# Kernel optimization log

Measured on AMD Instinct MI355X. Metric: run time of the kernel, lower is better.

Reference implementation:

```python
import jax, jax.numpy as jnp
import numpy as np

# Static module hyperparameters (from init_kwargs)
K = 4        # kernel_size
STRIDE = 2
L = 2        # n_layers
F = 4        # filters
NQ = 6       # n_qubits = ceil(log2(4*4*4)) = 6
D = 1 << NQ  # statevector dim = 64 = in_channels*K*K (no padding needed)

# Pauli-Z expectation sign table: wire 0 is the most-significant bit (PennyLane convention)
_bits = (jnp.arange(D)[None, :] >> (NQ - 1 - jnp.arange(NQ)[:, None])) & 1  # (NQ, D)
ZSIGNS = (1 - 2 * _bits).astype(jnp.float32)                                # (NQ, D)


def setup_inputs() -> dict:
    key = jax.random.key(0)
    k1, k2 = jax.random.split(key)
    x = jax.random.normal(k1, (128, 4, 64, 64), dtype=jnp.float32)
    weights = jax.random.normal(k2, (F, L, NQ, 3), dtype=jnp.float32)
    return {"x": x, "weights": weights}


def _rot_mat(phi, theta, omega):
    # qml.Rot = RZ(omega) @ RY(theta) @ RZ(phi)
    c = jnp.cos(theta / 2)
    s = jnp.sin(theta / 2)
    return jnp.stack([
        jnp.stack([jnp.exp(-1j * (phi + omega) / 2) * c, -jnp.exp(1j * (phi - omega) / 2) * s]),
        jnp.stack([jnp.exp(-1j * (phi - omega) / 2) * s, jnp.exp(1j * (phi + omega) / 2) * c]),
    ])  # (2,2) complex64


def _apply_1q(state, U, w):
    # state: (N, D) complex; apply 2x2 unitary on wire w (MSB-first ordering)
    N = state.shape[0]
    s = state.reshape(N, 1 << w, 2, 1 << (NQ - 1 - w))
    s = jnp.einsum('ij,najb->naib', U, s)
    return s.reshape(N, D)


def _apply_cnot(state, c, t):
    # flip target bit t where control bit c is 1
    N = state.shape[0]
    a, b = min(c, t), max(c, t)
    s = state.reshape(N, 1 << a, 2, 1 << (b - a - 1), 2, 1 << (NQ - 1 - b))
    if c < t:
        # control axis=2, target axis=4
        s = s.at[:, :, 1].set(s[:, :, 1, :, ::-1, :])
    else:
        # target axis=2, control axis=4
        s = s.at[:, :, :, :, 1, :].set(s[:, :, ::-1, :, 1, :])
    return s.reshape(N, D)


def _simulate(psi0, wf):
    # psi0: (N, D) complex64 normalized amplitudes; wf: (L, NQ, 3) float32
    state = psi0
    # The torch module applies StronglyEntanglingLayers(weights) L times -> L*L layers total.
    for _ in range(L):
        for l in range(L):
            for w in range(NQ):
                U = _rot_mat(wf[l, w, 0], wf[l, w, 1], wf[l, w, 2])
                state = _apply_1q(state, U, w)
            r = (l % (NQ - 1)) + 1  # StronglyEntanglingLayers default ranges
            for w in range(NQ):
                state = _apply_cnot(state, w, (w + r) % NQ)
    probs = state.real ** 2 + state.imag ** 2  # (N, D)
    return probs @ ZSIGNS.T                    # (N, NQ) Pauli-Z expvals


def reference(x, weights):
    B, C, H, W = x.shape
    oh = (H - K) // STRIDE + 1
    i = jnp.arange(oh) * STRIDE
    # vectorized sliding-window patch extraction, row-major (i outer, j inner)
    rows = x[:, :, i[:, None] + jnp.arange(K)[None, :], :]           # (B,C,oh,K,W)
    pat = rows[:, :, :, :, i[:, None] + jnp.arange(K)[None, :]]      # (B,C,oh,K,oh,K)
    pat = pat.transpose(0, 2, 4, 1, 3, 5).reshape(B, oh * oh, C * K * K)  # (B,P,D), flatten order (C,k,k)
    # AmplitudeEmbedding with normalize=True (C*K*K == 2**NQ, no padding)
    norm = jnp.linalg.norm(pat, axis=-1, keepdims=True)
    psi0 = (pat / norm).astype(jnp.complex64).reshape(-1, D)         # (B*P, D)
    exp = jax.vmap(lambda wf: _simulate(psi0, wf))(weights)          # (F, B*P, NQ)
    out = exp.reshape(F, B, oh * oh, NQ).transpose(1, 0, 3, 2).reshape(B, F * NQ, oh, oh)
    return out
```

## Files before the change

### kernel.cpp

```cpp
#include <hip/hip_runtime.h>

typedef float f32x2 __attribute__((ext_vector_type(2)));
typedef float f32x16 __attribute__((ext_vector_type(16)));
typedef __bf16 bf16x8 __attribute__((ext_vector_type(8)));

static __device__ __forceinline__ unsigned short f2bf(float v) {
    unsigned u = __builtin_bit_cast(unsigned, v);
    unsigned r = (u + 0x7FFFu + ((u >> 16) & 1u)) >> 16;
    return (unsigned short)r;
}
static __device__ __forceinline__ float bf2f(unsigned short h) {
    unsigned u = ((unsigned)h) << 16;
    return __builtin_bit_cast(float, u);
}
static __device__ __forceinline__ bf16x8 ldg8(const unsigned short* p) {
    uint4 u = *(const uint4*)p;
    return __builtin_bit_cast(bf16x8, u);
}
static __device__ __forceinline__ f32x16 mfma32(bf16x8 a, bf16x8 b, f32x16 c) {
    return __builtin_amdgcn_mfma_f32_32x32x16_bf16(a, b, c, 0, 0, 0);
}

__global__ __launch_bounds__(256) void prep_M(const float* __restrict__ wts,
                                              unsigned short* __restrict__ Mhi) {
    __shared__ float gls[12][8];
    const int f = blockIdx.x >> 4;
    const int tid = threadIdx.x;
    if (tid < 12) {
        int l = tid / 6, w = tid % 6;
        const float* p = wts + ((f * 2 + l) * 6 + w) * 3;
        float phi = p[0], theta = p[1], omega = p[2];
        float c, s; sincosf(0.5f * theta, &s, &c);
        float sapo, capo, samo, camo;
        sincosf(0.5f * (phi + omega), &sapo, &capo);
        sincosf(0.5f * (phi - omega), &samo, &camo);
        float* o = gls[tid];
        o[0] =  capo * c;  o[1] = -sapo * c;
        o[2] = -camo * s;  o[3] = -samo * s;
        o[4] =  camo * s;  o[5] = -samo * s;
        o[6] =  capo * c;  o[7] =  sapo * c;
    }
    __syncthreads();

    const int lane = tid & 63;
    const int wid  = tid >> 6;
    const int bas  = (blockIdx.x & 15) * 4 + wid;

    int src0 = lane, src1 = lane;
#pragma unroll
    for (int w = 5; w >= 0; --w) { int tq = (w + 1) % 6; src0 ^= ((src0 >> (5 - w)) & 1) << (5 - tq); }
#pragma unroll
    for (int w = 5; w >= 0; --w) { int tq = (w + 2) % 6; src1 ^= ((src1 >> (5 - w)) & 1) << (5 - tq); }

    float ar = (lane == bas) ? 1.0f : 0.0f, ai = 0.0f;
#pragma unroll
    for (int rep = 0; rep < 2; ++rep) {
#pragma unroll
        for (int l = 0; l < 2; ++l) {
#pragma unroll
            for (int w = 0; w < 6; ++w) {
                const float* gp = gls[l * 6 + w];
                const float4 uA = *(const float4*)gp;
                const float4 uB = *(const float4*)(gp + 4);
                const int m = 32 >> w;
                const float br = __shfl_xor(ar, m);
                const float bi = __shfl_xor(ai, m);
                const bool hi = (lane & m) != 0;
                const float cmr = hi ? uB.z : uA.x;
                const float cmi = hi ? uB.w : uA.y;
                const float cpr = hi ? uB.x : uA.z;
                const float cpi = hi ? uB.y : uA.w;
                const float nr = cmr * ar - cmi * ai + cpr * br - cpi * bi;
                const float ni = cmr * ai + cmi * ar + cpr * bi + cpi * br;
                ar = nr; ai = ni;
            }
            const int src = l ? src1 : src0;
            ar = __shfl(ar, src);
            ai = __shfl(ai, src);
        }
    }
    Mhi[((f * 2 + 0) * 64 + lane) * 64 + bas] = f2bf(ar);
    Mhi[((f * 2 + 1) * 64 + lane) * 64 + bas] = f2bf(ai);
}

__global__ __launch_bounds__(256, 4) void qconv_main(
        const float* __restrict__ x,
        const unsigned short* __restrict__ Mhi,
        float* __restrict__ out) {
    __shared__ __align__(16) unsigned char smem[12288];
    unsigned short* psiH = (unsigned short*)smem;
    float* zbuf = (float*)smem;

    const int tid  = threadIdx.x;
    const int lane = tid & 63;
    const int w    = tid >> 6;
    const int n0   = blockIdx.x * 64;

    {
        const int p = tid >> 2;
        const int q = tid & 3;
        const int n = n0 + p;
        const int b = n / 961, pos = n - b * 961;
        const int i = pos / 31, j = pos - i * 31;
        const float* base = x + (((b * 4 + q) * 64) + i * 2) * 64 + j * 2;
        float v[16];
#pragma unroll
        for (int kh = 0; kh < 4; ++kh) {
            const float* r = base + kh * 64;
            *(f32x2*)&v[kh * 4]     = *(const f32x2*)r;
            *(f32x2*)&v[kh * 4 + 2] = *(const f32x2*)(r + 2);
        }
        float ss = 0.f;
#pragma unroll
        for (int k = 0; k < 16; ++k) ss += v[k] * v[k];
        ss += __shfl_xor(ss, 1);
        ss += __shfl_xor(ss, 2);
        const float rn = rsqrtf(ss);
        unsigned hu[8];
#pragma unroll
        for (int k2 = 0; k2 < 8; ++k2) {
            __bf16 h0 = (__bf16)(v[2 * k2] * rn);
            __bf16 h1 = (__bf16)(v[2 * k2 + 1] * rn);
            hu[k2] = (unsigned)__builtin_bit_cast(unsigned short, h0)
                   | ((unsigned)__builtin_bit_cast(unsigned short, h1) << 16);
        }
        const int s0i = p * 64 + ((2 * q) ^ (p & 7)) * 8;
        const int s1i = p * 64 + ((2 * q + 1) ^ (p & 7)) * 8;
        *(uint4*)&psiH[s0i] = make_uint4(hu[0], hu[1], hu[2], hu[3]);
        *(uint4*)&psiH[s1i] = make_uint4(hu[4], hu[5], hu[6], hu[7]);
    }
    __syncthreads();

    bf16x8 Bh[2][4];
    {
        const int pc = lane & 31, hi = lane >> 5;
#pragma unroll
        for (int ct = 0; ct < 2; ++ct) {
            const int pp = ct * 32 + pc;
#pragma unroll
            for (int ks = 0; ks < 4; ++ks) {
                const int idx = pp * 64 + ((2 * ks + hi) ^ (pp & 7)) * 8;
                Bh[ct][ks] = __builtin_bit_cast(bf16x8, *(const uint4*)&psiH[idx]);
            }
        }
    }
    __syncthreads();

    const int arow = ((lane >> 4) & 1) * 4096 + (w * 16 + (lane & 15)) * 64 + (lane >> 5) * 8;
    const int hi5 = lane >> 5;

#pragma unroll 1
    for (int fp = 0; fp < 2; ++fp) {
        bf16x8 A8[2][4];
#pragma unroll
        for (int fo = 0; fo < 2; ++fo) {
            const int off = (fp * 2 + fo) * 8192 + arow;
#pragma unroll
            for (int ks = 0; ks < 4; ++ks) A8[fo][ks] = ldg8(Mhi + off + ks * 16);
        }
#pragma unroll
        for (int fo = 0; fo < 2; ++fo) {
            f32x16 C0, C1;
#pragma unroll
            for (int r = 0; r < 16; ++r) { C0[r] = 0.f; C1[r] = 0.f; }
#pragma unroll
            for (int ks = 0; ks < 4; ++ks) {
                C0 = mfma32(A8[fo][ks], Bh[0][ks], C0);
                C1 = mfma32(A8[fo][ks], Bh[1][ks], C1);
            }
#pragma unroll
            for (int ct = 0; ct < 2; ++ct) {
                const f32x16 Cv = ct ? C1 : C0;
                float P[8];
#pragma unroll
                for (int r = 0; r < 8; ++r) P[r] = Cv[r] * Cv[r] + Cv[r + 8] * Cv[r + 8];
                const float e0 = P[0] + P[1], o0 = P[0] - P[1];
                const float e1 = P[2] + P[3], o1 = P[2] - P[3];
                const float e2 = P[4] + P[5], o2 = P[4] - P[5];
                const float e3 = P[6] + P[7], o3 = P[6] - P[7];
                const float s01 = e0 + e1, s23 = e2 + e3;
                float S  = s01 + s23;
                float Z2 = s01 - s23;
                float Z4 = (e0 - e1) + (e2 - e3);
                float Z5 = o0 + o1 + o2 + o3;
                float Z3 = hi5 ? -S : S;
                S  += __shfl_xor(S, 32);
                Z2 += __shfl_xor(Z2, 32);
                Z3 += __shfl_xor(Z3, 32);
                Z4 += __shfl_xor(Z4, 32);
                Z5 += __shfl_xor(Z5, 32);
                if (lane < 32) {
                    const int pp = ct * 32 + lane;
                    zbuf[((fo * 6 + 0) * 4 + w) * 64 + pp] = (w & 2) ? -S : S;
                    zbuf[((fo * 6 + 1) * 4 + w) * 64 + pp] = (w & 1) ? -S : S;
                    zbuf[((fo * 6 + 2) * 4 + w) * 64 + pp] = Z2;
                    zbuf[((fo * 6 + 3) * 4 + w) * 64 + pp] = Z3;
                    zbuf[((fo * 6 + 4) * 4 + w) * 64 + pp] = Z4;
                    zbuf[((fo * 6 + 5) * 4 + w) * 64 + pp] = Z5;
                }
            }
        }
        __syncthreads();
#pragma unroll 1
        for (int u = tid; u < 768; u += 256) {
            const int fo  = u / 384;
            const int rem = u - fo * 384;
            const int q   = rem >> 6;
            const int p   = rem & 63;
            const int zb  = (fo * 6 + q) * 4 * 64 + p;
            const float sum = zbuf[zb] + zbuf[zb + 64] + zbuf[zb + 128] + zbuf[zb + 192];
            const int f = fp * 2 + fo;
            const int n = n0 + p;
            const int b = n / 961, pos = n - b * 961;
            out[(b * 24 + f * 6 + q) * 961 + pos] = sum;
        }
        __syncthreads();
    }
}

extern "C" void kernel_launch(void* const* d_in, const int* in_sizes, int n_in,
                              void* d_out, int out_size, void* d_ws, size_t ws_size,
                              hipStream_t stream) {
    const float* x   = (const float*)d_in[0];
    const float* wts = (const float*)d_in[1];
    float* out = (float*)d_out;

    unsigned short* Mhi = (unsigned short*)d_ws;

    prep_M<<<64, 256, 0, stream>>>(wts, Mhi);

    const int npatch = 128 * 31 * 31;
    qconv_main<<<npatch / 64, 256, 0, stream>>>(x, Mhi, out);
}
```

Before: 32.11 us.

## Give each wave its own 32 patches and drop shared-memory staging and reductions

Each wavefront now owns 32 patches and loads them straight from global memory into MFMA B-fragments. It loops over all four row quarters of the M matrix and accumulates the Z expectations in registers. This removes the LDS staging of normalized amplitudes, the cross-wave zbuf reduction and all __syncthreads. Each block now covers 128 patches instead of 64, which halves the grid. In exchange every wave reloads the full M matrix (four times more global/L2 traffic for M per wave), and there are fewer blocks to spread across the device.

```diff
diff --git a/kernel.cpp b/kernel.cpp
--- a/kernel.cpp
+++ b/kernel.cpp
@@ -8,10 +8,6 @@
     unsigned u = __builtin_bit_cast(unsigned, v);
     unsigned r = (u + 0x7FFFu + ((u >> 16) & 1u)) >> 16;
     return (unsigned short)r;
-}
-static __device__ __forceinline__ float bf2f(unsigned short h) {
-    unsigned u = ((unsigned)h) << 16;
-    return __builtin_bit_cast(float, u);
 }
 static __device__ __forceinline__ bf16x8 ldg8(const unsigned short* p) {
     uint4 u = *(const uint4*)p;
@@ -87,90 +83,70 @@
         const float* __restrict__ x,
         const unsigned short* __restrict__ Mhi,
         float* __restrict__ out) {
-    __shared__ __align__(16) unsigned char smem[12288];
-    unsigned short* psiH = (unsigned short*)smem;
-    float* zbuf = (float*)smem;
-
     const int tid  = threadIdx.x;
     const int lane = tid & 63;
     const int w    = tid >> 6;
-    const int n0   = blockIdx.x * 64;
-
-    {
-        const int p = tid >> 2;
-        const int q = tid & 3;
-        const int n = n0 + p;
-        const int b = n / 961, pos = n - b * 961;
-        const int i = pos / 31, j = pos - i * 31;
-        const float* base = x + (((b * 4 + q) * 64) + i * 2) * 64 + j * 2;
-        float v[16];
-#pragma unroll
-        for (int kh = 0; kh < 4; ++kh) {
-            const float* r = base + kh * 64;
-            *(f32x2*)&v[kh * 4]     = *(const f32x2*)r;
-            *(f32x2*)&v[kh * 4 + 2] = *(const f32x2*)(r + 2);
-        }
-        float ss = 0.f;
-#pragma unroll
-        for (int k = 0; k < 16; ++k) ss += v[k] * v[k];
-        ss += __shfl_xor(ss, 1);
-        ss += __shfl_xor(ss, 2);
-        const float rn = rsqrtf(ss);
-        unsigned hu[8];
-#pragma unroll
-        for (int k2 = 0; k2 < 8; ++k2) {
-            __bf16 h0 = (__bf16)(v[2 * k2] * rn);
-            __bf16 h1 = (__bf16)(v[2 * k2 + 1] * rn);
-            hu[k2] = (unsigned)__builtin_bit_cast(unsigned short, h0)
-                   | ((unsigned)__builtin_bit_cast(unsigned short, h1) << 16);
-        }
-        const int s0i = p * 64 + ((2 * q) ^ (p & 7)) * 8;
-        const int s1i = p * 64 + ((2 * q + 1) ^ (p & 7)) * 8;
-        *(uint4*)&psiH[s0i] = make_uint4(hu[0], hu[1], hu[2], hu[3]);
-        *(uint4*)&psiH[s1i] = make_uint4(hu[4], hu[5], hu[6], hu[7]);
-    }
-    __syncthreads();
-
-    bf16x8 Bh[2][4];
-    {
-        const int pc = lane & 31, hi = lane >> 5;
-#pragma unroll
-        for (int ct = 0; ct < 2; ++ct) {
-            const int pp = ct * 32 + pc;
-#pragma unroll
-            for (int ks = 0; ks < 4; ++ks) {
-                const int idx = pp * 64 + ((2 * ks + hi) ^ (pp & 7)) * 8;
-                Bh[ct][ks] = __builtin_bit_cast(bf16x8, *(const uint4*)&psiH[idx]);
-            }
-        }
-    }
-    __syncthreads();
-
-    const int arow = ((lane >> 4) & 1) * 4096 + (w * 16 + (lane & 15)) * 64 + (lane >> 5) * 8;
-    const int hi5 = lane >> 5;
+    const int pc   = lane & 31;
+    const int hi5  = lane >> 5;
+
+    const int n   = blockIdx.x * 128 + w * 32 + pc;
+    const int b   = n / 961;
+    const int pos = n - b * 961;
+    const int i   = pos / 31;
+    const int j   = pos - i * 31;
+
+    float v[4][8];
+    const float* xb = x + ((b * 4) * 64 + (i * 2 + hi5 * 2)) * 64 + j * 2;
+#pragma unroll
+    for (int ch = 0; ch < 4; ++ch) {
+        const float* r0 = xb + ch * 4096;
+        *(f32x2*)&v[ch][0] = *(const f32x2*)r0;
+        *(f32x2*)&v[ch][2] = *(const f32x2*)(r0 + 2);
+        *(f32x2*)&v[ch][4] = *(const f32x2*)(r0 + 64);
+        *(f32x2*)&v[ch][6] = *(const f32x2*)(r0 + 66);
+    }
+    float ss = 0.f;
+#pragma unroll
+    for (int ch = 0; ch < 4; ++ch)
+#pragma unroll
+        for (int k = 0; k < 8; ++k) ss += v[ch][k] * v[ch][k];
+    ss += __shfl_xor(ss, 32);
+    const float rn = rsqrtf(ss);
+
+    bf16x8 B[4];
+#pragma unroll
+    for (int ch = 0; ch < 4; ++ch)
+#pragma unroll
+        for (int k = 0; k < 8; ++k) B[ch][k] = (__bf16)(v[ch][k] * rn);
+
+    const int abase = ((lane >> 4) & 1) * 4096 + (lane & 15) * 64 + hi5 * 8;
+    float* const obase = out + b * 24 * 961 + pos;
 
 #pragma unroll 1
     for (int fp = 0; fp < 2; ++fp) {
-        bf16x8 A8[2][4];
-#pragma unroll
-        for (int fo = 0; fo < 2; ++fo) {
-            const int off = (fp * 2 + fo) * 8192 + arow;
-#pragma unroll
-            for (int ks = 0; ks < 4; ++ks) A8[fo][ks] = ldg8(Mhi + off + ks * 16);
-        }
-#pragma unroll
-        for (int fo = 0; fo < 2; ++fo) {
+        float zS0 = 0.f, za0 = 0.f, zb0 = 0.f, z20 = 0.f, z40 = 0.f, z50 = 0.f;
+        float zS1 = 0.f, za1 = 0.f, zb1 = 0.f, z21 = 0.f, z41 = 0.f, z51 = 0.f;
+#pragma unroll
+        for (int dq = 0; dq < 4; ++dq) {
+            const int off0 = (fp * 2 + 0) * 8192 + abase + dq * 1024;
+            const int off1 = (fp * 2 + 1) * 8192 + abase + dq * 1024;
+            bf16x8 Aa[4], Ab[4];
+#pragma unroll
+            for (int ks = 0; ks < 4; ++ks) {
+                Aa[ks] = ldg8(Mhi + off0 + ks * 16);
+                Ab[ks] = ldg8(Mhi + off1 + ks * 16);
+            }
             f32x16 C0, C1;
 #pragma unroll
             for (int r = 0; r < 16; ++r) { C0[r] = 0.f; C1[r] = 0.f; }
 #pragma unroll
             for (int ks = 0; ks < 4; ++ks) {
-                C0 = mfma32(A8[fo][ks], Bh[0][ks], C0);
-                C1 = mfma32(A8[fo][ks], Bh[1][ks], C1);
-            }
-#pragma unroll
-            for (int ct = 0; ct < 2; ++ct) {
-                const f32x16 Cv = ct ? C1 : C0;
+                C0 = mfma32(Aa[ks], B[ks], C0);
+                C1 = mfma32(Ab[ks], B[ks], C1);
+            }
+#pragma unroll
+            for (int fo = 0; fo < 2; ++fo) {
+                const f32x16 Cv = fo ? C1 : C0;
                 float P[8];
 #pragma unroll
                 for (int r = 0; r < 8; ++r) P[r] = Cv[r] * Cv[r] + Cv[r + 8] * Cv[r + 8];
@@ -179,42 +155,49 @@
                 const float e2 = P[4] + P[5], o2 = P[4] - P[5];
                 const float e3 = P[6] + P[7], o3 = P[6] - P[7];
                 const float s01 = e0 + e1, s23 = e2 + e3;
-                float S  = s01 + s23;
-                float Z2 = s01 - s23;
-                float Z4 = (e0 - e1) + (e2 - e3);
-                float Z5 = o0 + o1 + o2 + o3;
-                float Z3 = hi5 ? -S : S;
-                S  += __shfl_xor(S, 32);
-                Z2 += __shfl_xor(Z2, 32);
-                Z3 += __shfl_xor(Z3, 32);
-                Z4 += __shfl_xor(Z4, 32);
-                Z5 += __shfl_xor(Z5, 32);
-                if (lane < 32) {
-                    const int pp = ct * 32 + lane;
-                    zbuf[((fo * 6 + 0) * 4 + w) * 64 + pp] = (w & 2) ? -S : S;
-                    zbuf[((fo * 6 + 1) * 4 + w) * 64 + pp] = (w & 1) ? -S : S;
-                    zbuf[((fo * 6 + 2) * 4 + w) * 64 + pp] = Z2;
-                    zbuf[((fo * 6 + 3) * 4 + w) * 64 + pp] = Z3;
-                    zbuf[((fo * 6 + 4) * 4 + w) * 64 + pp] = Z4;
-                    zbuf[((fo * 6 + 5) * 4 + w) * 64 + pp] = Z5;
+                const float S  = s01 + s23;
+                const float Z2 = s01 - s23;
+                const float Z4 = (e0 - e1) + (e2 - e3);
+                const float Z5 = o0 + o1 + o2 + o3;
+                if (fo == 0) {
+                    zS0 += S;
+                    za0 += (dq & 2) ? -S : S;
+                    zb0 += (dq & 1) ? -S : S;
+                    z20 += Z2; z40 += Z4; z50 += Z5;
+                } else {
+                    zS1 += S;
+                    za1 += (dq & 2) ? -S : S;
+                    zb1 += (dq & 1) ? -S : S;
+                    z21 += Z2; z41 += Z4; z51 += Z5;
                 }
             }
         }
-        __syncthreads();
-#pragma unroll 1
-        for (int u = tid; u < 768; u += 256) {
-            const int fo  = u / 384;
-            const int rem = u - fo * 384;
-            const int q   = rem >> 6;
-            const int p   = rem & 63;
-            const int zb  = (fo * 6 + q) * 4 * 64 + p;
-            const float sum = zbuf[zb] + zbuf[zb + 64] + zbuf[zb + 128] + zbuf[zb + 192];
-            const int f = fp * 2 + fo;
-            const int n = n0 + p;
-            const int b = n / 961, pos = n - b * 961;
-            out[(b * 24 + f * 6 + q) * 961 + pos] = sum;
+#pragma unroll
+        for (int fo = 0; fo < 2; ++fo) {
+            float z0 = fo ? za1 : za0;
+            float z1 = fo ? zb1 : zb0;
+            float z2 = fo ? z21 : z20;
+            float zS = fo ? zS1 : zS0;
+            float z4 = fo ? z41 : z40;
+            float z5 = fo ? z51 : z50;
+            float z3 = hi5 ? -zS : zS;
+            z0 += __shfl_xor(z0, 32);
+            z1 += __shfl_xor(z1, 32);
+            z2 += __shfl_xor(z2, 32);
+            z3 += __shfl_xor(z3, 32);
+            z4 += __shfl_xor(z4, 32);
+            z5 += __shfl_xor(z5, 32);
+            float* o = obase + (fp * 2 + fo) * 6 * 961;
+            if (hi5 == 0) {
+                o[0]        = z0;
+                o[961]      = z1;
+                o[2 * 961]  = z2;
+            } else {
+                o[3 * 961]  = z3;
+                o[4 * 961]  = z4;
+                o[5 * 961]  = z5;
+            }
         }
-        __syncthreads();
     }
 }
 
@@ -230,5 +213,5 @@
     prep_M<<<64, 256, 0, stream>>>(wts, Mhi);
 
     const int npatch = 128 * 31 * 31;
-    qconv_main<<<npatch / 64, 256, 0, stream>>>(x, Mhi, out);
-}
+    qconv_main<<<npatch / 128, 256, 0, stream>>>(x, Mhi, out);
+}
```

Measured after the change: 55.34 us. 1.72x slower.

## Assign one filter per wavefront and accumulate Z expectations in registers

Applied to the files above, without the earlier changes.

Work is split so that each of the four wavefronts handles one whole filter and loops over the four 16-row groups of the 64-row output. The Pauli-Z partial sums now accumulate in registers, which removes the per-fp loop, the two extra block barriers and the cross-wave zbuf reduction; zbuf is written once and stored directly to global memory. The first half of the A fragments is also prefetched from global memory before the barrier that follows psi staging, so those loads overlap the barrier wait. LDS use grows slightly because psiH and zbuf no longer alias, and register pressure rises from the prefetched fragments.

```diff
diff --git a/kernel.cpp b/kernel.cpp
--- a/kernel.cpp
+++ b/kernel.cpp
@@ -8,10 +8,6 @@
     unsigned u = __builtin_bit_cast(unsigned, v);
     unsigned r = (u + 0x7FFFu + ((u >> 16) & 1u)) >> 16;
     return (unsigned short)r;
-}
-static __device__ __forceinline__ float bf2f(unsigned short h) {
-    unsigned u = ((unsigned)h) << 16;
-    return __builtin_bit_cast(float, u);
 }
 static __device__ __forceinline__ bf16x8 ldg8(const unsigned short* p) {
     uint4 u = *(const uint4*)p;
@@ -87,9 +83,8 @@
         const float* __restrict__ x,
         const unsigned short* __restrict__ Mhi,
         float* __restrict__ out) {
-    __shared__ __align__(16) unsigned char smem[12288];
-    unsigned short* psiH = (unsigned short*)smem;
-    float* zbuf = (float*)smem;
+    __shared__ __align__(16) unsigned short psiH[4096];
+    __shared__ float zbuf[4][6][64];
 
     const int tid  = threadIdx.x;
     const int lane = tid & 63;
@@ -129,92 +124,112 @@
         *(uint4*)&psiH[s0i] = make_uint4(hu[0], hu[1], hu[2], hu[3]);
         *(uint4*)&psiH[s1i] = make_uint4(hu[4], hu[5], hu[6], hu[7]);
     }
+
+    const int hi5   = lane >> 5;
+    const int abase = ((lane >> 4) & 1) * 4096 + (lane & 15) * 64 + hi5 * 8;
+    const int foff  = w * 8192;
+
+    bf16x8 Apre[2][4];
+#pragma unroll
+    for (int dd = 0; dd < 2; ++dd)
+#pragma unroll
+        for (int ks = 0; ks < 4; ++ks)
+            Apre[dd][ks] = ldg8(Mhi + foff + abase + dd * 1024 + ks * 16);
+
     __syncthreads();
 
     bf16x8 Bh[2][4];
     {
-        const int pc = lane & 31, hi = lane >> 5;
+        const int pc = lane & 31;
 #pragma unroll
         for (int ct = 0; ct < 2; ++ct) {
             const int pp = ct * 32 + pc;
 #pragma unroll
             for (int ks = 0; ks < 4; ++ks) {
-                const int idx = pp * 64 + ((2 * ks + hi) ^ (pp & 7)) * 8;
+                const int idx = pp * 64 + ((2 * ks + hi5) ^ (pp & 7)) * 8;
                 Bh[ct][ks] = __builtin_bit_cast(bf16x8, *(const uint4*)&psiH[idx]);
             }
         }
     }
+
+    float zS[2] = {0.f, 0.f}, za[2] = {0.f, 0.f}, zbq[2] = {0.f, 0.f};
+    float z2[2] = {0.f, 0.f}, z4[2] = {0.f, 0.f}, z5[2] = {0.f, 0.f};
+
+#pragma unroll
+    for (int dq = 0; dq < 4; ++dq) {
+        bf16x8 A[4];
+        if (dq < 2) {
+#pragma unroll
+            for (int ks = 0; ks < 4; ++ks) A[ks] = Apre[dq][ks];
+        } else {
+#pragma unroll
+            for (int ks = 0; ks < 4; ++ks)
+                A[ks] = ldg8(Mhi + foff + abase + dq * 1024 + ks * 16);
+        }
+        f32x16 C0, C1;
+#pragma unroll
+        for (int r = 0; r < 16; ++r) { C0[r] = 0.f; C1[r] = 0.f; }
+#pragma unroll
+        for (int ks = 0; ks < 4; ++ks) {
+            C0 = mfma32(A[ks], Bh[0][ks], C0);
+            C1 = mfma32(A[ks], Bh[1][ks], C1);
+        }
+#pragma unroll
+        for (int ct = 0; ct < 2; ++ct) {
+            const f32x16 Cv = ct ? C1 : C0;
+            float P[8];
+#pragma unroll
+            for (int r = 0; r < 8; ++r) P[r] = Cv[r] * Cv[r] + Cv[r + 8] * Cv[r + 8];
+            const float e0 = P[0] + P[1], o0 = P[0] - P[1];
+            const float e1 = P[2] + P[3], o1 = P[2] - P[3];
+            const float e2 = P[4] + P[5], o2 = P[4] - P[5];
+            const float e3 = P[6] + P[7], o3 = P[6] - P[7];
+            const float s01 = e0 + e1, s23 = e2 + e3;
+            const float S  = s01 + s23;
+            zS[ct]  += S;
+            za[ct]  += (dq & 2) ? -S : S;
+            zbq[ct] += (dq & 1) ? -S : S;
+            z2[ct]  += s01 - s23;
+            z4[ct]  += (e0 - e1) + (e2 - e3);
+            z5[ct]  += o0 + o1 + o2 + o3;
+        }
+    }
+
+#pragma unroll
+    for (int ct = 0; ct < 2; ++ct) {
+        float t0 = za[ct];
+        float t1 = zbq[ct];
+        float t2 = z2[ct];
+        float t3 = hi5 ? -zS[ct] : zS[ct];
+        float t4 = z4[ct];
+        float t5 = z5[ct];
+        t0 += __shfl_xor(t0, 32);
+        t1 += __shfl_xor(t1, 32);
+        t2 += __shfl_xor(t2, 32);
+        t3 += __shfl_xor(t3, 32);
+        t4 += __shfl_xor(t4, 32);
+        t5 += __shfl_xor(t5, 32);
+        const int pp = ct * 32 + (lane & 31);
+        if (hi5 == 0) {
+            zbuf[w][0][pp] = t0;
+            zbuf[w][1][pp] = t1;
+            zbuf[w][2][pp] = t2;
+        } else {
+            zbuf[w][3][pp] = t3;
+            zbuf[w][4][pp] = t4;
+            zbuf[w][5][pp] = t5;
+        }
+    }
     __syncthreads();
 
-    const int arow = ((lane >> 4) & 1) * 4096 + (w * 16 + (lane & 15)) * 64 + (lane >> 5) * 8;
-    const int hi5 = lane >> 5;
-
-#pragma unroll 1
-    for (int fp = 0; fp < 2; ++fp) {
-        bf16x8 A8[2][4];
-#pragma unroll
-        for (int fo = 0; fo < 2; ++fo) {
-            const int off = (fp * 2 + fo) * 8192 + arow;
-#pragma unroll
-            for (int ks = 0; ks < 4; ++ks) A8[fo][ks] = ldg8(Mhi + off + ks * 16);
-        }
-#pragma unroll
-        for (int fo = 0; fo < 2; ++fo) {
-            f32x16 C0, C1;
-#pragma unroll
-            for (int r = 0; r < 16; ++r) { C0[r] = 0.f; C1[r] = 0.f; }
-#pragma unroll
-            for (int ks = 0; ks < 4; ++ks) {
-                C0 = mfma32(A8[fo][ks], Bh[0][ks], C0);
-                C1 = mfma32(A8[fo][ks], Bh[1][ks], C1);
-            }
-#pragma unroll
-            for (int ct = 0; ct < 2; ++ct) {
-                const f32x16 Cv = ct ? C1 : C0;
-                float P[8];
-#pragma unroll
-                for (int r = 0; r < 8; ++r) P[r] = Cv[r] * Cv[r] + Cv[r + 8] * Cv[r + 8];
-                const float e0 = P[0] + P[1], o0 = P[0] - P[1];
-                const float e1 = P[2] + P[3], o1 = P[2] - P[3];
-                const float e2 = P[4] + P[5], o2 = P[4] - P[5];
-                const float e3 = P[6] + P[7], o3 = P[6] - P[7];
-                const float s01 = e0 + e1, s23 = e2 + e3;
-                float S  = s01 + s23;
-                float Z2 = s01 - s23;
-                float Z4 = (e0 - e1) + (e2 - e3);
-                float Z5 = o0 + o1 + o2 + o3;
-                float Z3 = hi5 ? -S : S;
-                S  += __shfl_xor(S, 32);
-                Z2 += __shfl_xor(Z2, 32);
-                Z3 += __shfl_xor(Z3, 32);
-                Z4 += __shfl_xor(Z4, 32);
-                Z5 += __shfl_xor(Z5, 32);
-                if (lane < 32) {
-                    const int pp = ct * 32 + lane;
-                    zbuf[((fo * 6 + 0) * 4 + w) * 64 + pp] = (w & 2) ? -S : S;
-                    zbuf[((fo * 6 + 1) * 4 + w) * 64 + pp] = (w & 1) ? -S : S;
-                    zbuf[((fo * 6 + 2) * 4 + w) * 64 + pp] = Z2;
-                    zbuf[((fo * 6 + 3) * 4 + w) * 64 + pp] = Z3;
-                    zbuf[((fo * 6 + 4) * 4 + w) * 64 + pp] = Z4;
-                    zbuf[((fo * 6 + 5) * 4 + w) * 64 + pp] = Z5;
-                }
-            }
-        }
-        __syncthreads();
-#pragma unroll 1
-        for (int u = tid; u < 768; u += 256) {
-            const int fo  = u / 384;
-            const int rem = u - fo * 384;
-            const int q   = rem >> 6;
-            const int p   = rem & 63;
-            const int zb  = (fo * 6 + q) * 4 * 64 + p;
-            const float sum = zbuf[zb] + zbuf[zb + 64] + zbuf[zb + 128] + zbuf[zb + 192];
-            const int f = fp * 2 + fo;
-            const int n = n0 + p;
-            const int b = n / 961, pos = n - b * 961;
-            out[(b * 24 + f * 6 + q) * 961 + pos] = sum;
-        }
-        __syncthreads();
+#pragma unroll
+    for (int u = tid; u < 1536; u += 256) {
+        const int m = u >> 6;
+        const int p = u & 63;
+        const float zv = ((const float*)zbuf)[u];
+        const int n = n0 + p;
+        const int b = n / 961, pos = n - b * 961;
+        out[(b * 24 + m) * 961 + pos] = zv;
     }
 }
 
```

Measured after the change: 38.73 us. 20.6% more time.

## Process two patch tiles per block so each loaded circuit matrix feeds twice the MFMAs

Applied to the files above, without the earlier changes.

Each block now handles two 64-patch tiles, one from batch images 0-63 and one from 64-127, and computes them against the same per-filter matrix fragments. The loop runs over single filters with four accumulators instead of filter pairs. This halves the global loads of the matrix per patch and the block count, and removes the separate zbuf reuse of the psi buffer. In exchange it uses more registers and LDS, with launch bounds lowered to 3 blocks per CU, and the grid of 961 blocks may fill the machine less evenly.

```diff
diff --git a/kernel.cpp b/kernel.cpp
--- a/kernel.cpp
+++ b/kernel.cpp
@@ -8,10 +8,6 @@
     unsigned u = __builtin_bit_cast(unsigned, v);
     unsigned r = (u + 0x7FFFu + ((u >> 16) & 1u)) >> 16;
     return (unsigned short)r;
-}
-static __device__ __forceinline__ float bf2f(unsigned short h) {
-    unsigned u = ((unsigned)h) << 16;
-    return __builtin_bit_cast(float, u);
 }
 static __device__ __forceinline__ bf16x8 ldg8(const unsigned short* p) {
     uint4 u = *(const uint4*)p;
@@ -83,94 +79,100 @@
     Mhi[((f * 2 + 1) * 64 + lane) * 64 + bas] = f2bf(ai);
 }
 
-__global__ __launch_bounds__(256, 4) void qconv_main(
+__global__ __launch_bounds__(256, 3) void qconv_main(
         const float* __restrict__ x,
         const unsigned short* __restrict__ Mhi,
         float* __restrict__ out) {
-    __shared__ __align__(16) unsigned char smem[12288];
-    unsigned short* psiH = (unsigned short*)smem;
-    float* zbuf = (float*)smem;
+    __shared__ __align__(16) unsigned short psiH[2][4096];
+    __shared__ float zbuf[2][6][4][64];
 
     const int tid  = threadIdx.x;
     const int lane = tid & 63;
     const int w    = tid >> 6;
-    const int n0   = blockIdx.x * 64;
+    const int bid  = blockIdx.x;
 
     {
         const int p = tid >> 2;
         const int q = tid & 3;
-        const int n = n0 + p;
-        const int b = n / 961, pos = n - b * 961;
+        const int n = bid * 64 + p;
+        const int b0 = n / 961, pos = n - b0 * 961;
         const int i = pos / 31, j = pos - i * 31;
-        const float* base = x + (((b * 4 + q) * 64) + i * 2) * 64 + j * 2;
-        float v[16];
-#pragma unroll
-        for (int kh = 0; kh < 4; ++kh) {
-            const float* r = base + kh * 64;
-            *(f32x2*)&v[kh * 4]     = *(const f32x2*)r;
-            *(f32x2*)&v[kh * 4 + 2] = *(const f32x2*)(r + 2);
-        }
-        float ss = 0.f;
-#pragma unroll
-        for (int k = 0; k < 16; ++k) ss += v[k] * v[k];
-        ss += __shfl_xor(ss, 1);
-        ss += __shfl_xor(ss, 2);
-        const float rn = rsqrtf(ss);
-        unsigned hu[8];
-#pragma unroll
-        for (int k2 = 0; k2 < 8; ++k2) {
-            __bf16 h0 = (__bf16)(v[2 * k2] * rn);
-            __bf16 h1 = (__bf16)(v[2 * k2 + 1] * rn);
-            hu[k2] = (unsigned)__builtin_bit_cast(unsigned short, h0)
-                   | ((unsigned)__builtin_bit_cast(unsigned short, h1) << 16);
-        }
-        const int s0i = p * 64 + ((2 * q) ^ (p & 7)) * 8;
-        const int s1i = p * 64 + ((2 * q + 1) ^ (p & 7)) * 8;
-        *(uint4*)&psiH[s0i] = make_uint4(hu[0], hu[1], hu[2], hu[3]);
-        *(uint4*)&psiH[s1i] = make_uint4(hu[4], hu[5], hu[6], hu[7]);
+        const float* base0 = x + (((b0 * 4 + q) * 64) + i * 2) * 64 + j * 2;
+        float v[2][16];
+#pragma unroll
+        for (int t = 0; t < 2; ++t) {
+            const float* base = base0 + t * 64 * 4 * 64 * 64;
+#pragma unroll
+            for (int kh = 0; kh < 4; ++kh) {
+                const float* r = base + kh * 64;
+                *(f32x2*)&v[t][kh * 4]     = *(const f32x2*)r;
+                *(f32x2*)&v[t][kh * 4 + 2] = *(const f32x2*)(r + 2);
+            }
+        }
+#pragma unroll
+        for (int t = 0; t < 2; ++t) {
+            float ss = 0.f;
+#pragma unroll
+            for (int k = 0; k < 16; ++k) ss += v[t][k] * v[t][k];
+            ss += __shfl_xor(ss, 1);
+            ss += __shfl_xor(ss, 2);
+            const float rn = rsqrtf(ss);
+            unsigned hu[8];
+#pragma unroll
+            for (int k2 = 0; k2 < 8; ++k2) {
+                __bf16 h0 = (__bf16)(v[t][2 * k2] * rn);
+                __bf16 h1 = (__bf16)(v[t][2 * k2 + 1] * rn);
+                hu[k2] = (unsigned)__builtin_bit_cast(unsigned short, h0)
+                       | ((unsigned)__builtin_bit_cast(unsigned short, h1) << 16);
+            }
+            const int s0i = p * 64 + ((2 * q) ^ (p & 7)) * 8;
+            const int s1i = p * 64 + ((2 * q + 1) ^ (p & 7)) * 8;
+            *(uint4*)&psiH[t][s0i] = make_uint4(hu[0], hu[1], hu[2], hu[3]);
+            *(uint4*)&psiH[t][s1i] = make_uint4(hu[4], hu[5], hu[6], hu[7]);
+        }
     }
     __syncthreads();
 
-    bf16x8 Bh[2][4];
-    {
-        const int pc = lane & 31, hi = lane >> 5;
+    bf16x8 Bh[2][2][4];
+    const int pc  = lane & 31;
+    const int hi5 = lane >> 5;
+#pragma unroll
+    for (int t = 0; t < 2; ++t) {
 #pragma unroll
         for (int ct = 0; ct < 2; ++ct) {
             const int pp = ct * 32 + pc;
 #pragma unroll
             for (int ks = 0; ks < 4; ++ks) {
-                const int idx = pp * 64 + ((2 * ks + hi) ^ (pp & 7)) * 8;
-                Bh[ct][ks] = __builtin_bit_cast(bf16x8, *(const uint4*)&psiH[idx]);
-            }
-        }
-    }
-    __syncthreads();
-
-    const int arow = ((lane >> 4) & 1) * 4096 + (w * 16 + (lane & 15)) * 64 + (lane >> 5) * 8;
-    const int hi5 = lane >> 5;
+                const int idx = pp * 64 + ((2 * ks + hi5) ^ (pp & 7)) * 8;
+                Bh[t][ct][ks] = __builtin_bit_cast(bf16x8, *(const uint4*)&psiH[t][idx]);
+            }
+        }
+    }
+
+    const int arow = ((lane >> 4) & 1) * 4096 + (w * 16 + (lane & 15)) * 64 + hi5 * 8;
 
 #pragma unroll 1
-    for (int fp = 0; fp < 2; ++fp) {
-        bf16x8 A8[2][4];
-#pragma unroll
-        for (int fo = 0; fo < 2; ++fo) {
-            const int off = (fp * 2 + fo) * 8192 + arow;
-#pragma unroll
-            for (int ks = 0; ks < 4; ++ks) A8[fo][ks] = ldg8(Mhi + off + ks * 16);
-        }
-#pragma unroll
-        for (int fo = 0; fo < 2; ++fo) {
-            f32x16 C0, C1;
-#pragma unroll
-            for (int r = 0; r < 16; ++r) { C0[r] = 0.f; C1[r] = 0.f; }
-#pragma unroll
-            for (int ks = 0; ks < 4; ++ks) {
-                C0 = mfma32(A8[fo][ks], Bh[0][ks], C0);
-                C1 = mfma32(A8[fo][ks], Bh[1][ks], C1);
-            }
+    for (int f = 0; f < 4; ++f) {
+        bf16x8 A[4];
+#pragma unroll
+        for (int ks = 0; ks < 4; ++ks) A[ks] = ldg8(Mhi + f * 8192 + arow + ks * 16);
+
+        f32x16 C00, C01, C10, C11;
+#pragma unroll
+        for (int r = 0; r < 16; ++r) { C00[r] = 0.f; C01[r] = 0.f; C10[r] = 0.f; C11[r] = 0.f; }
+#pragma unroll
+        for (int ks = 0; ks < 4; ++ks) {
+            C00 = mfma32(A[ks], Bh[0][0][ks], C00);
+            C01 = mfma32(A[ks], Bh[0][1][ks], C01);
+            C10 = mfma32(A[ks], Bh[1][0][ks], C10);
+            C11 = mfma32(A[ks], Bh[1][1][ks], C11);
+        }
+
+#pragma unroll
+        for (int t = 0; t < 2; ++t) {
 #pragma unroll
             for (int ct = 0; ct < 2; ++ct) {
-                const f32x16 Cv = ct ? C1 : C0;
+                const f32x16 Cv = t ? (ct ? C11 : C10) : (ct ? C01 : C00);
                 float P[8];
 #pragma unroll
                 for (int r = 0; r < 8; ++r) P[r] = Cv[r] * Cv[r] + Cv[r + 8] * Cv[r + 8];
@@ -191,28 +193,30 @@
                 Z5 += __shfl_xor(Z5, 32);
                 if (lane < 32) {
                     const int pp = ct * 32 + lane;
-                    zbuf[((fo * 6 + 0) * 4 + w) * 64 + pp] = (w & 2) ? -S : S;
-                    zbuf[((fo * 6 + 1) * 4 + w) * 64 + pp] = (w & 1) ? -S : S;
-                    zbuf[((fo * 6 + 2) * 4 + w) * 64 + pp] = Z2;
-                    zbuf[((fo * 6 + 3) * 4 + w) * 64 + pp] = Z3;
-                    zbuf[((fo * 6 + 4) * 4 + w) * 64 + pp] = Z4;
-                    zbuf[((fo * 6 + 5) * 4 + w) * 64 + pp] = Z5;
+                    zbuf[t][0][w][pp] = (w & 2) ? -S : S;
+                    zbuf[t][1][w][pp] = (w & 1) ? -S : S;
+                    zbuf[t][2][w][pp] = Z2;
+                    zbuf[t][3][w][pp] = Z3;
+                    zbuf[t][4][w][pp] = Z4;
+                    zbuf[t][5][w][pp] = Z5;
                 }
             }
         }
         __syncthreads();
-#pragma unroll 1
+
+#pragma unroll
         for (int u = tid; u < 768; u += 256) {
-            const int fo  = u / 384;
-            const int rem = u - fo * 384;
+            const int t   = u / 384;
+            const int rem = u - t * 384;
             const int q   = rem >> 6;
             const int p   = rem & 63;
-            const int zb  = (fo * 6 + q) * 4 * 64 + p;
-            const float sum = zbuf[zb] + zbuf[zb + 64] + zbuf[zb + 128] + zbuf[zb + 192];
-            const int f = fp * 2 + fo;
-            const int n = n0 + p;
-            const int b = n / 961, pos = n - b * 961;
-            out[(b * 24 + f * 6 + q) * 961 + pos] = sum;
+            const float* zb = &zbuf[t][q][0][p];
+            const float sum = zb[0] + zb[64] + zb[128] + zb[192];
+            const int nn = bid * 64 + p;
+            int bb = nn / 961;
+            const int pos = nn - bb * 961;
+            bb += t * 64;
+            out[(bb * 24 + f * 6 + q) * 961 + pos] = sum;
         }
         __syncthreads();
     }
@@ -229,6 +233,5 @@
 
     prep_M<<<64, 256, 0, stream>>>(wts, Mhi);
 
-    const int npatch = 128 * 31 * 31;
-    qconv_main<<<npatch / 64, 256, 0, stream>>>(x, Mhi, out);
-}
+    qconv_main<<<961, 256, 0, stream>>>(x, Mhi, out);
+}
```

Measured after the change: 30.22 us. -5.9%, faster.
